# Kernel optimization log

Hardware: AMD Instinct MI355X
Metric: run time of the kernel (lower is better)

The kernel has to match this reference:

```python
import jax, jax.numpy as jnp
import numpy as np

HEAD_DIM = 64
EMBED_DIM = 1024

def setup_inputs() -> dict:
    key = jax.random.key(0)
    k1, k2, k3, k4 = jax.random.split(key, 4)
    x = jax.random.normal(k1, (4, 4096, EMBED_DIM), dtype=jnp.float32)
    # nn.Linear(embed_dim, head_dim, bias=False): weight shape (head_dim, embed_dim)
    s = 1.0 / np.sqrt(EMBED_DIM)
    Wq = jax.random.uniform(k2, (HEAD_DIM, EMBED_DIM), jnp.float32, -s, s)
    Wk = jax.random.uniform(k3, (HEAD_DIM, EMBED_DIM), jnp.float32, -s, s)
    Wv = jax.random.uniform(k4, (HEAD_DIM, EMBED_DIM), jnp.float32, -s, s)
    return {"x": x, "Wq": Wq, "Wk": Wk, "Wv": Wv}

def reference(x, Wq, Wk, Wv):
    # Faithful to source: V = self.key(x), i.e. uses Wk (Wv is an unused param).
    n_ctx = x.shape[1]
    Q = jnp.einsum('bse,de->bsd', x, Wq)
    K = jnp.einsum('bse,de->bsd', x, Wk)
    V = jnp.einsum('bse,de->bsd', x, Wk)
    scale = 1.0 / jnp.sqrt(jnp.asarray(K.shape[-1], x.dtype))
    scores = jnp.einsum('bqd,bkd->bqk', Q, K) * scale  # [b, n_ctx, n_ctx]
    causal = jnp.tril(jnp.ones((n_ctx, n_ctx), dtype=bool))
    scores = jnp.where(causal, scores, jnp.asarray(-jnp.inf, scores.dtype))
    attn = jax.nn.softmax(scores, axis=-1)
    # dropout(p=0.2) omitted: reference runs in eval mode (identity)
    out = jnp.einsum('bqk,bkd->bqd', attn, V)
    return out
```

## Files before the change

### kernel.cpp

```cpp
#include <hip/hip_runtime.h>

typedef _Float16 f16;
typedef _Float16 f16x8 __attribute__((ext_vector_type(8)));
typedef _Float16 f16x4 __attribute__((ext_vector_type(4)));
typedef float f32x4 __attribute__((ext_vector_type(4)));

#define S_LEN 4096
#define B_SZ  4
#define E_DIM 1024
#define D_DIM 64
#define NROWS (B_SZ * S_LEN)
#define NSPLIT 4
#define QSCALE (0.125f * 1.44269504088896f)
#define SMAX 8.0f

__device__ __forceinline__ float exp2g(float x) { return __builtin_amdgcn_exp2f(x); }

__global__ __launch_bounds__(256) void wpack_kernel(const float* __restrict__ Wq,
                                                    const float* __restrict__ Wk,
                                                    f16* __restrict__ Bp) {
    int id = blockIdx.x * 256 + threadIdx.x;
    int lane = id & 63, kc = (id >> 6) & 31, n = id >> 11;
    int row = n * 16 + (lane & 15);
    int col = kc * 32 + (lane >> 4) * 8;
    const float* src = (row < 64) ? (Wq + (long)row * E_DIM + col)
                                  : (Wk + (long)(row - 64) * E_DIM + col);
    float4 v0 = ((const float4*)src)[0];
    float4 v1 = ((const float4*)src)[1];
    f16x8 h = {(f16)v0.x, (f16)v0.y, (f16)v0.z, (f16)v0.w,
               (f16)v1.x, (f16)v1.y, (f16)v1.z, (f16)v1.w};
    *(f16x8*)(Bp + (long)id * 8) = h;
}

__global__ __launch_bounds__(256, 4) void proj_kernel(const float* __restrict__ x,
                                                      const f16* __restrict__ Bp,
                                                      f16* __restrict__ Qh,
                                                      f16* __restrict__ Kh) {
    __shared__ union {
        f16   xs[16][1040];
        float rb[4][16][132];
    } sm;

    const int tid  = threadIdx.x;
    const int w    = tid >> 6;
    const int lane = tid & 63;
    const int l15  = lane & 15;
    const int quad = lane >> 4;
    const long m0  = (long)blockIdx.x * 16;

#pragma unroll
    for (int c = 0; c < 16; c++) {
        int f4 = c * 256 + tid;
        int row = f4 >> 8;
        int col = (f4 & 255) * 4;
        float4 v = *(const float4*)(x + (m0 + row) * E_DIM + col);
        f16x4 h = {(f16)v.x, (f16)v.y, (f16)v.z, (f16)v.w};
        *(f16x4*)&sm.xs[row][col] = h;
    }
    __syncthreads();

    f32x4 acc[8];
#pragma unroll
    for (int n = 0; n < 8; n++) acc[n] = (f32x4){0.f, 0.f, 0.f, 0.f};

    const int kc0 = w * 8;
#pragma unroll
    for (int s = 0; s < 8; s++) {
        f16x8 a = *(const f16x8*)&sm.xs[l15][w * 256 + s * 32 + quad * 8];
#pragma unroll
        for (int n = 0; n < 8; n++) {
            f16x8 b = *(const f16x8*)(Bp + (((long)n * 32 + kc0 + s) * 64 + lane) * 8);
            acc[n] = __builtin_amdgcn_mfma_f32_16x16x32_f16(a, b, acc[n], 0, 0, 0);
        }
    }
    __syncthreads();

#pragma unroll
    for (int n = 0; n < 8; n++)
#pragma unroll
        for (int r = 0; r < 4; r++)
            sm.rb[w][quad * 4 + r][n * 16 + l15] = acc[n][r];
    __syncthreads();

    const int row = tid >> 4;
    const int c0  = (tid & 15) * 8;
    float sum[8];
#pragma unroll
    for (int i = 0; i < 8; i++) sum[i] = 0.f;
#pragma unroll
    for (int w4 = 0; w4 < 4; w4++)
#pragma unroll
        for (int g = 0; g < 2; g++) {
            f32x4 u = *(const f32x4*)&sm.rb[w4][row][c0 + g * 4];
#pragma unroll
            for (int i = 0; i < 4; i++) sum[g * 4 + i] += u[i];
        }

    const long grow = m0 + row;
    f16 tmp[8];
    if (c0 < 64) {
#pragma unroll
        for (int i = 0; i < 8; i++) tmp[i] = (f16)(sum[i] * QSCALE);
        *(f16x8*)(Qh + grow * 64 + c0) = *(f16x8*)tmp;
    } else {
#pragma unroll
        for (int i = 0; i < 8; i++) tmp[i] = (f16)sum[i];
        *(f16x8*)(Kh + grow * 64 + (c0 - 64)) = *(f16x8*)tmp;
    }
}

__global__ __launch_bounds__(256, 4) void attn_kernel(const f16* __restrict__ Qh,
                                                      const f16* __restrict__ Kh,
                                                      float* __restrict__ OutP0,
                                                      f16* __restrict__ P123,
                                                      float* __restrict__ Ml) {
    __shared__ __align__(16) f16 Kr[64][72];
    __shared__ __align__(16) f16 Kt[64][72];
    __shared__ __align__(16) f16 Pm[64][88];

    const int tid  = threadIdx.x;
    const int w    = tid >> 6;
    const int lane = tid & 63;
    const int l15  = lane & 15;
    const int quad = lane >> 4;

    const int bid  = blockIdx.x;
    const int qraw = bid & 63;
    const int half = (bid >> 6) & 3;
    const int b    = bid >> 8;
    const int qt   = (b & 1) ? (63 - qraw) : qraw;
    const long q0  = (long)qt * 64;

    const f16* Qb = Qh + (long)b * S_LEN * 64;
    const f16* Kb = Kh + (long)b * S_LEN * 64;

    f16x8 Aq[2];
#pragma unroll
    for (int kf = 0; kf < 2; kf++)
        Aq[kf] = *(const f16x8*)(Qb + (q0 + w * 16 + l15) * 64 + kf * 32 + quad * 8);

    const f16x8 ones = {(f16)1.f, (f16)1.f, (f16)1.f, (f16)1.f,
                        (f16)1.f, (f16)1.f, (f16)1.f, (f16)1.f};

    f32x4 O[4];
    f32x4 Lacc = (f32x4){0.f, 0.f, 0.f, 0.f};
#pragma unroll
    for (int n = 0; n < 4; n++) O[n] = (f32x4){0.f, 0.f, 0.f, 0.f};

    f16x8 pre[2];
    if (half <= qt) {
#pragma unroll
        for (int it = 0; it < 2; it++)
            pre[it] = *(const f16x8*)(Kb + ((long)half * 64 + lane) * 64 + (w + it * 4) * 8);
    }

    for (int j = half; j <= qt; j += NSPLIT) {
        __syncthreads();
#pragma unroll
        for (int it = 0; it < 2; it++) {
            int sg = w + it * 4;
            *(f16x8*)&Kr[lane][sg * 8] = pre[it];
#pragma unroll
            for (int i = 0; i < 8; i++) Kt[sg * 8 + i][lane] = pre[it][i];
        }
        if (j + NSPLIT <= qt) {
#pragma unroll
            for (int it = 0; it < 2; it++)
                pre[it] = *(const f16x8*)(Kb + ((long)(j + NSPLIT) * 64 + lane) * 64 + (w + it * 4) * 8);
        }
        __syncthreads();

        f32x4 S[4];
#pragma unroll
        for (int n = 0; n < 4; n++) S[n] = (f32x4){0.f, 0.f, 0.f, 0.f};
#pragma unroll
        for (int n = 0; n < 4; n++)
#pragma unroll
            for (int kf = 0; kf < 2; kf++) {
                f16x8 bfr = *(const f16x8*)&Kr[n * 16 + l15][kf * 32 + quad * 8];
                S[n] = __builtin_amdgcn_mfma_f32_16x16x32_f16(Aq[kf], bfr, S[n], 0, 0, 0);
            }

        if (j == qt) {
#pragma unroll
            for (int n = 0; n < 4; n++) {
                int col_rel = n * 16 + l15;
#pragma unroll
                for (int r = 0; r < 4; r++)
                    if (col_rel > w * 16 + quad * 4 + r) S[n][r] = -1e30f;
            }
        }

#pragma unroll
        for (int n = 0; n < 4; n++)
#pragma unroll
            for (int r = 0; r < 4; r++)
                Pm[w * 16 + quad * 4 + r][n * 16 + l15] = (f16)exp2g(S[n][r] - SMAX);

#pragma unroll
        for (int kf = 0; kf < 2; kf++) {
            f16x8 pa = *(const f16x8*)&Pm[w * 16 + l15][kf * 32 + quad * 8];
            Lacc = __builtin_amdgcn_mfma_f32_16x16x32_f16(pa, ones, Lacc, 0, 0, 0);
#pragma unroll
            for (int n = 0; n < 4; n++) {
                f16x8 vb = *(const f16x8*)&Kt[n * 16 + l15][kf * 32 + quad * 8];
                O[n] = __builtin_amdgcn_mfma_f32_16x16x32_f16(pa, vb, O[n], 0, 0, 0);
            }
        }
    }

    const long growbase = (long)b * S_LEN + q0;
#pragma unroll
    for (int r = 0; r < 4; r++) {
        long grow = growbase + w * 16 + quad * 4 + r;
        if (half == 0) {
#pragma unroll
            for (int n = 0; n < 4; n++) OutP0[grow * 64 + n * 16 + l15] = O[n][r];
        } else {
            f16* dst = P123 + (long)(half - 1) * NROWS * 64;
#pragma unroll
            for (int n = 0; n < 4; n++) dst[grow * 64 + n * 16 + l15] = (f16)O[n][r];
        }
        if (l15 == 0) Ml[(long)half * NROWS + grow] = Lacc[r];
    }
}

__global__ __launch_bounds__(256) void combine_kernel(float* __restrict__ Out,
                                                      const f16* __restrict__ P123,
                                                      const float* __restrict__ Ml) {
    int gid = blockIdx.x * 256 + threadIdx.x;
    long row = gid >> 4;
    int c0 = (gid & 15) * 4;
    float lt = 0.f;
#pragma unroll
    for (int h = 0; h < 4; h++) lt += Ml[(long)h * NROWS + row];
    float inv = 1.0f / lt;

    float* p = Out + row * 64 + c0;
    float4 res = *(const float4*)p;
#pragma unroll
    for (int h = 1; h < 4; h++) {
        f16x4 oh = *(const f16x4*)(P123 + (long)(h - 1) * NROWS * 64 + row * 64 + c0);
        res.x += (float)oh[0];
        res.y += (float)oh[1];
        res.z += (float)oh[2];
        res.w += (float)oh[3];
    }
    *(float4*)p = make_float4(res.x * inv, res.y * inv, res.z * inv, res.w * inv);
}

extern "C" void kernel_launch(void* const* d_in, const int* in_sizes, int n_in,
                              void* d_out, int out_size, void* d_ws, size_t ws_size,
                              hipStream_t stream) {
    const float* x  = (const float*)d_in[0];
    const float* Wq = (const float*)d_in[1];
    const float* Wk = (const float*)d_in[2];
    float* out = (float*)d_out;

    f16* Qh    = (f16*)d_ws;
    f16* Kh    = Qh + (long)NROWS * D_DIM;
    f16* Bp    = Kh + (long)NROWS * D_DIM;
    f16* P123  = Bp + (long)128 * E_DIM;
    float* Ml  = (float*)(P123 + 3L * NROWS * D_DIM);

    wpack_kernel<<<dim3(64), dim3(256), 0, stream>>>(Wq, Wk, Bp);
    proj_kernel<<<dim3(NROWS / 16), dim3(256), 0, stream>>>(x, Bp, Qh, Kh);
    attn_kernel<<<dim3(64 * NSPLIT * B_SZ), dim3(256), 0, stream>>>(Qh, Kh, out, P123, Ml);
    combine_kernel<<<dim3(NROWS * 16 / 256), dim3(256), 0, stream>>>(out, P123, Ml);
}
```

Baseline: 134.8 us.

## Pre-pack K into MFMA fragment layout and run attention per-wave without LDS

Adds a kpack kernel that rewrites K into two fragment-ordered layouts, one for the QK^T operand and one transposed for the PV operand. Each wave of the attention kernel then handles its own 16-row query tile and KV split, reading fragments straight from global memory with no LDS staging and no block barriers. Computing S transposed lets P stay in registers as the A operand of 16x16x16 MFMAs. The cost is an extra pass and extra workspace for the packed copies, more global and L2 traffic because each wave reloads K instead of sharing it, and a finer causal-work granularity.

```diff
diff --git a/kernel.cpp b/kernel.cpp
--- a/kernel.cpp
+++ b/kernel.cpp
@@ -109,119 +109,131 @@
     }
 }
 
-__global__ __launch_bounds__(256, 4) void attn_kernel(const f16* __restrict__ Qh,
-                                                      const f16* __restrict__ Kh,
-                                                      float* __restrict__ OutP0,
-                                                      f16* __restrict__ P123,
-                                                      float* __restrict__ Ml) {
-    __shared__ __align__(16) f16 Kr[64][72];
-    __shared__ __align__(16) f16 Kt[64][72];
-    __shared__ __align__(16) f16 Pm[64][88];
-
+__global__ __launch_bounds__(256) void kpack_kernel(const f16* __restrict__ Kh,
+                                                    f16* __restrict__ Khp,
+                                                    f16* __restrict__ Kvp) {
+    __shared__ __align__(16) f16 T[64][72];
+    const int tid  = threadIdx.x;
+    const int lane = tid & 63;
+    const int l15  = lane & 15;
+    const int quad = lane >> 4;
+    const int g    = tid >> 6;
+    const int b    = blockIdx.x >> 6;
+    const int c    = blockIdx.x & 63;
+    const f16* src = Kh + ((long)b * S_LEN + c * 64) * 64;
+
+    {
+        int s = tid >> 2;
+        int col = (tid & 3) * 16;
+        f16x8 v0 = *(const f16x8*)(src + s * 64 + col);
+        f16x8 v1 = *(const f16x8*)(src + s * 64 + col + 8);
+        *(f16x8*)&T[s][col]     = v0;
+        *(f16x8*)&T[s][col + 8] = v1;
+    }
+    __syncthreads();
+
+    {
+        int t = g;
+#pragma unroll
+        for (int kf = 0; kf < 2; kf++) {
+            f16x8 v = *(const f16x8*)&T[t * 16 + l15][kf * 32 + quad * 8];
+            *(f16x8*)(Khp + ((((long)b * 64 + c) * 4 + t) * 2 + kf) * 512 + lane * 8) = v;
+        }
+    }
+#pragma unroll
+    for (int c2 = 0; c2 < 4; c2++) {
+        int combo = g * 4 + c2;
+        int t = combo >> 2, n = combo & 3;
+        f16 tmp[4];
+#pragma unroll
+        for (int j = 0; j < 4; j++)
+            tmp[j] = T[t * 16 + quad * 4 + j][n * 16 + l15];
+        *(f16x4*)(Kvp + ((((long)b * 64 + c) * 4 + t) * 4 + n) * 256 + lane * 4) = *(f16x4*)tmp;
+    }
+}
+
+__global__ __launch_bounds__(256) void attn_kernel(const f16* __restrict__ Qh,
+                                                   const f16* __restrict__ Khp,
+                                                   const f16* __restrict__ Kvp,
+                                                   float* __restrict__ OutP0,
+                                                   f16* __restrict__ P123,
+                                                   float* __restrict__ Ml) {
     const int tid  = threadIdx.x;
     const int w    = tid >> 6;
     const int lane = tid & 63;
     const int l15  = lane & 15;
     const int quad = lane >> 4;
 
-    const int bid  = blockIdx.x;
-    const int qraw = bid & 63;
-    const int half = (bid >> 6) & 3;
-    const int b    = bid >> 8;
-    const int qt   = (b & 1) ? (63 - qraw) : qraw;
-    const long q0  = (long)qt * 64;
+    const int gw  = blockIdx.x * 4 + w;
+    const int h   = gw & 3;
+    const int q16 = (gw >> 2) & 255;
+    const int b   = gw >> 10;
+    const int q0  = q16 * 16;
+    const int jmax = q16 >> 2;
 
     const f16* Qb = Qh + (long)b * S_LEN * 64;
-    const f16* Kb = Kh + (long)b * S_LEN * 64;
-
     f16x8 Aq[2];
 #pragma unroll
     for (int kf = 0; kf < 2; kf++)
-        Aq[kf] = *(const f16x8*)(Qb + (q0 + w * 16 + l15) * 64 + kf * 32 + quad * 8);
-
-    const f16x8 ones = {(f16)1.f, (f16)1.f, (f16)1.f, (f16)1.f,
-                        (f16)1.f, (f16)1.f, (f16)1.f, (f16)1.f};
-
+        Aq[kf] = *(const f16x8*)(Qb + (long)(q0 + l15) * 64 + kf * 32 + quad * 8);
+
+    const f16x4 ones = {(f16)1.f, (f16)1.f, (f16)1.f, (f16)1.f};
     f32x4 O[4];
     f32x4 Lacc = (f32x4){0.f, 0.f, 0.f, 0.f};
 #pragma unroll
     for (int n = 0; n < 4; n++) O[n] = (f32x4){0.f, 0.f, 0.f, 0.f};
 
-    f16x8 pre[2];
-    if (half <= qt) {
-#pragma unroll
-        for (int it = 0; it < 2; it++)
-            pre[it] = *(const f16x8*)(Kb + ((long)half * 64 + lane) * 64 + (w + it * 4) * 8);
-    }
-
-    for (int j = half; j <= qt; j += NSPLIT) {
-        __syncthreads();
-#pragma unroll
-        for (int it = 0; it < 2; it++) {
-            int sg = w + it * 4;
-            *(f16x8*)&Kr[lane][sg * 8] = pre[it];
-#pragma unroll
-            for (int i = 0; i < 8; i++) Kt[sg * 8 + i][lane] = pre[it][i];
-        }
-        if (j + NSPLIT <= qt) {
-#pragma unroll
-            for (int it = 0; it < 2; it++)
-                pre[it] = *(const f16x8*)(Kb + ((long)(j + NSPLIT) * 64 + lane) * 64 + (w + it * 4) * 8);
-        }
-        __syncthreads();
-
-        f32x4 S[4];
-#pragma unroll
-        for (int n = 0; n < 4; n++) S[n] = (f32x4){0.f, 0.f, 0.f, 0.f};
+    for (int j = h; j <= jmax; j += NSPLIT) {
+        const f16* ka = Khp + ((long)b * 64 + j) * 4096 + lane * 8;
+        const f16* kv = Kvp + ((long)b * 64 + j) * 4096 + lane * 4;
+
+        f16x4 P[4];
+#pragma unroll
+        for (int t = 0; t < 4; t++) {
+            f32x4 St = (f32x4){0.f, 0.f, 0.f, 0.f};
+#pragma unroll
+            for (int kf = 0; kf < 2; kf++) {
+                f16x8 Ak = *(const f16x8*)(ka + (t * 2 + kf) * 512);
+                St = __builtin_amdgcn_mfma_f32_16x16x32_f16(Ak, Aq[kf], St, 0, 0, 0);
+            }
+            if (j == jmax) {
+                int kc = j * 64 + t * 16 + quad * 4;
+                int qr = q0 + l15;
+#pragma unroll
+                for (int r = 0; r < 4; r++)
+                    if (kc + r > qr) St[r] = -1e30f;
+            }
+#pragma unroll
+            for (int r = 0; r < 4; r++)
+                P[t][r] = (f16)exp2g(St[r] - SMAX);
+        }
+
+#pragma unroll
+        for (int t = 0; t < 4; t++)
+            Lacc = __builtin_amdgcn_mfma_f32_16x16x16f16(P[t], ones, Lacc, 0, 0, 0);
+
 #pragma unroll
         for (int n = 0; n < 4; n++)
 #pragma unroll
-            for (int kf = 0; kf < 2; kf++) {
-                f16x8 bfr = *(const f16x8*)&Kr[n * 16 + l15][kf * 32 + quad * 8];
-                S[n] = __builtin_amdgcn_mfma_f32_16x16x32_f16(Aq[kf], bfr, S[n], 0, 0, 0);
+            for (int t = 0; t < 4; t++) {
+                f16x4 Bv = *(const f16x4*)(kv + (t * 4 + n) * 256);
+                O[n] = __builtin_amdgcn_mfma_f32_16x16x16f16(P[t], Bv, O[n], 0, 0, 0);
             }
-
-        if (j == qt) {
-#pragma unroll
-            for (int n = 0; n < 4; n++) {
-                int col_rel = n * 16 + l15;
-#pragma unroll
-                for (int r = 0; r < 4; r++)
-                    if (col_rel > w * 16 + quad * 4 + r) S[n][r] = -1e30f;
-            }
-        }
-
-#pragma unroll
-        for (int n = 0; n < 4; n++)
-#pragma unroll
-            for (int r = 0; r < 4; r++)
-                Pm[w * 16 + quad * 4 + r][n * 16 + l15] = (f16)exp2g(S[n][r] - SMAX);
-
-#pragma unroll
-        for (int kf = 0; kf < 2; kf++) {
-            f16x8 pa = *(const f16x8*)&Pm[w * 16 + l15][kf * 32 + quad * 8];
-            Lacc = __builtin_amdgcn_mfma_f32_16x16x32_f16(pa, ones, Lacc, 0, 0, 0);
-#pragma unroll
-            for (int n = 0; n < 4; n++) {
-                f16x8 vb = *(const f16x8*)&Kt[n * 16 + l15][kf * 32 + quad * 8];
-                O[n] = __builtin_amdgcn_mfma_f32_16x16x32_f16(pa, vb, O[n], 0, 0, 0);
-            }
-        }
     }
 
     const long growbase = (long)b * S_LEN + q0;
 #pragma unroll
     for (int r = 0; r < 4; r++) {
-        long grow = growbase + w * 16 + quad * 4 + r;
-        if (half == 0) {
+        long grow = growbase + quad * 4 + r;
+        if (h == 0) {
 #pragma unroll
             for (int n = 0; n < 4; n++) OutP0[grow * 64 + n * 16 + l15] = O[n][r];
         } else {
-            f16* dst = P123 + (long)(half - 1) * NROWS * 64;
+            f16* dst = P123 + (long)(h - 1) * NROWS * 64;
 #pragma unroll
             for (int n = 0; n < 4; n++) dst[grow * 64 + n * 16 + l15] = (f16)O[n][r];
         }
-        if (l15 == 0) Ml[(long)half * NROWS + grow] = Lacc[r];
+        if (l15 == 0) Ml[(long)h * NROWS + grow] = Lacc[r];
     }
 }
 
@@ -257,14 +269,17 @@
     const float* Wk = (const float*)d_in[2];
     float* out = (float*)d_out;
 
-    f16* Qh    = (f16*)d_ws;
-    f16* Kh    = Qh + (long)NROWS * D_DIM;
-    f16* Bp    = Kh + (long)NROWS * D_DIM;
-    f16* P123  = Bp + (long)128 * E_DIM;
-    float* Ml  = (float*)(P123 + 3L * NROWS * D_DIM);
+    f16* Qh   = (f16*)d_ws;
+    f16* Kh   = Qh + (long)NROWS * D_DIM;
+    f16* Bp   = Kh + (long)NROWS * D_DIM;
+    f16* Khp  = Bp + (long)128 * E_DIM;
+    f16* Kvp  = Khp + (long)NROWS * D_DIM;
+    f16* P123 = Kvp + (long)NROWS * D_DIM;
+    float* Ml = (float*)(P123 + 3L * NROWS * D_DIM);
 
     wpack_kernel<<<dim3(64), dim3(256), 0, stream>>>(Wq, Wk, Bp);
     proj_kernel<<<dim3(NROWS / 16), dim3(256), 0, stream>>>(x, Bp, Qh, Kh);
-    attn_kernel<<<dim3(64 * NSPLIT * B_SZ), dim3(256), 0, stream>>>(Qh, Kh, out, P123, Ml);
+    kpack_kernel<<<dim3(B_SZ * 64), dim3(256), 0, stream>>>(Kh, Khp, Kvp);
+    attn_kernel<<<dim3(B_SZ * 256 * NSPLIT / 4), dim3(256), 0, stream>>>(Qh, Khp, Kvp, out, P123, Ml);
     combine_kernel<<<dim3(NROWS * 16 / 256), dim3(256), 0, stream>>>(out, P123, Ml);
 }
```

After: 163.0 us. 20.9% more time.
